# Performance work log

Measured on AMD Instinct MI355X. Metric: run time of the kernel, lower is better.

The kernel has to match this reference:

```python
import jax, jax.numpy as jnp
import numpy as np

TOPK_FALLBACK = 12  # hard-coded k in the torch source


def setup_inputs() -> dict:
    key = jax.random.key(0)
    k1, k2 = jax.random.split(key)
    bs, C, H, W = 16, 256, 128, 128
    feature_q = jax.random.normal(k1, (bs, C, H, W), dtype=jnp.float32)
    out = jax.random.normal(k2, (bs, 2, H, W), dtype=jnp.float32)
    tau = jnp.asarray(0.5, dtype=jnp.float32)  # learned threshold parameter
    return {"feature_q": feature_q, "out": out, "tau": tau}


def _proto(feat, p, thres):
    # feat: [bs, C, N], p: [bs, N] probabilities, thres: scalar
    mask = (p > thres).astype(feat.dtype)            # [bs, N]
    cnt = mask.sum(axis=-1)                          # [bs]
    # masked mean over spatial positions (single fused reduction pass)
    masked_mean = jnp.einsum('bcn,bn->bc', feat, mask) / jnp.maximum(cnt, 1.0)[:, None]
    # branchless top-k fallback when no position passes the threshold
    _, idx = jax.lax.top_k(p, TOPK_FALLBACK)         # [bs, k]
    topk_mean = jnp.take_along_axis(feat, idx[:, None, :], axis=2).mean(axis=-1)  # [bs, C]
    return jnp.where((cnt > 0)[:, None], masked_mean, topk_mean)


def reference(feature_q, out, tau):
    bs, C = feature_q.shape[0], feature_q.shape[1]
    pred = jax.nn.softmax(out.reshape(bs, 2, -1), axis=1)  # [bs, 2, N]
    pred_fg, pred_bg = pred[:, 1], pred[:, 0]
    feat = feature_q.reshape(bs, C, -1)                    # [bs, C, N]
    fg_thres = jax.nn.sigmoid(tau)
    bg_thres = 1.0 - fg_thres
    fg_proto = _proto(feat, pred_fg, fg_thres)[:, :, None, None]  # [bs, C, 1, 1]
    bg_proto = _proto(feat, pred_bg, bg_thres)[:, :, None, None]
    return fg_proto, bg_proto
```

## Files before the change

kernel.cpp:

```cpp
#include <hip/hip_runtime.h>
#include <math.h>

#define BS   16
#define CH   256
#define NPIX 16384
#define TOPK 12

__global__ __launch_bounds__(256) void mask_kernel(
    const float* __restrict__ outp,
    const float* __restrict__ tau,
    unsigned char* __restrict__ masks,
    int* __restrict__ cnts)
{
    int b = blockIdx.x >> 6;
    int n = ((blockIdx.x & 63) << 8) + threadIdx.x;

    float t = tau[0];
    float fthres = 1.0f / (1.0f + expf(-t));
    float bthres = 1.0f - fthres;

    float o0 = outp[((size_t)b * 2    ) * NPIX + n];
    float o1 = outp[((size_t)b * 2 + 1) * NPIX + n];
    float m  = fmaxf(o0, o1);
    float e0 = expf(o0 - m);
    float e1 = expf(o1 - m);
    float inv = 1.0f / (e0 + e1);
    float pf = e1 * inv;
    float pb = e0 * inv;

    int fg = pf > fthres ? 1 : 0;
    int bg = pb > bthres ? 1 : 0;
    masks[((size_t)b << 14) + n] = (unsigned char)(fg | (bg << 1));

    unsigned long long balf = __ballot(fg);
    unsigned long long balb = __ballot(bg);
    if ((threadIdx.x & 63) == 0) {
        atomicAdd(&cnts[b],      (int)__popcll(balf));
        atomicAdd(&cnts[BS + b], (int)__popcll(balb));
    }
}

__global__ __launch_bounds__(256) void sum_kernel(
    const float* __restrict__ feat,
    const unsigned char* __restrict__ masks,
    float* __restrict__ dout)
{
    int b = blockIdx.x >> 8;
    int c = blockIdx.x & (CH - 1);

    const float4* fp = (const float4*)(feat + (((size_t)b * CH + c) << 14));
    const uchar4* mp = (const uchar4*)(masks + ((size_t)b << 14));

    float sfg = 0.0f, sbg = 0.0f;
    #pragma unroll
    for (int i = 0; i < 16; ++i) {
        int idx = i * 256 + threadIdx.x;
        float4 f = fp[idx];
        uchar4 mm = mp[idx];
        if (mm.x & 1) sfg += f.x;
        if (mm.y & 1) sfg += f.y;
        if (mm.z & 1) sfg += f.z;
        if (mm.w & 1) sfg += f.w;
        if (mm.x & 2) sbg += f.x;
        if (mm.y & 2) sbg += f.y;
        if (mm.z & 2) sbg += f.z;
        if (mm.w & 2) sbg += f.w;
    }

    #pragma unroll
    for (int off = 32; off > 0; off >>= 1) {
        sfg += __shfl_down(sfg, off);
        sbg += __shfl_down(sbg, off);
    }
    __shared__ float shf[4], shb[4];
    int lane = threadIdx.x & 63, wid = threadIdx.x >> 6;
    if (lane == 0) { shf[wid] = sfg; shb[wid] = sbg; }
    __syncthreads();
    if (threadIdx.x == 0) {
        float tf = shf[0] + shf[1] + shf[2] + shf[3];
        float tb = shb[0] + shb[1] + shb[2] + shb[3];
        dout[b * CH + c]           = tf;
        dout[BS * CH + b * CH + c] = tb;
    }
}

__global__ __launch_bounds__(256) void finalize_kernel(
    const float* __restrict__ feat,
    const float* __restrict__ outp,
    const float* __restrict__ tau,
    const int* __restrict__ cnts,
    float* __restrict__ dout)
{
    int b     = blockIdx.x >> 1;
    int which = blockIdx.x & 1;
    int cnt   = cnts[which * BS + b];
    float* o  = dout + (size_t)which * BS * CH + (size_t)b * CH;

    if (cnt > 0) {
        o[threadIdx.x] = o[threadIdx.x] / (float)cnt;
        return;
    }

    __shared__ int   sel[TOPK];
    __shared__ float shv[256];
    __shared__ int   shi[256];

    const float* o0p = outp + ((size_t)b * 2) * NPIX;
    const float* o1p = o0p + NPIX;

    for (int k = 0; k < TOPK; ++k) {
        float bestv = -INFINITY;
        int   besti = 0x7fffffff;
        for (int n = threadIdx.x; n < NPIX; n += 256) {
            bool skip = false;
            for (int j = 0; j < k; ++j) if (sel[j] == n) { skip = true; break; }
            if (skip) continue;
            float a0 = o0p[n], a1 = o1p[n];
            float m  = fmaxf(a0, a1);
            float e0 = expf(a0 - m);
            float e1 = expf(a1 - m);
            float p  = (which == 0 ? e1 : e0) / (e0 + e1);
            if (p > bestv || (p == bestv && n < besti)) { bestv = p; besti = n; }
        }
        shv[threadIdx.x] = bestv;
        shi[threadIdx.x] = besti;
        __syncthreads();
        for (int off = 128; off > 0; off >>= 1) {
            if (threadIdx.x < off) {
                float v2 = shv[threadIdx.x + off];
                int   i2 = shi[threadIdx.x + off];
                if (v2 > shv[threadIdx.x] ||
                    (v2 == shv[threadIdx.x] && i2 < shi[threadIdx.x])) {
                    shv[threadIdx.x] = v2;
                    shi[threadIdx.x] = i2;
                }
            }
            __syncthreads();
        }
        if (threadIdx.x == 0) sel[k] = shi[0];
        __syncthreads();
    }

    const float* fb = feat + ((size_t)b * CH + threadIdx.x) * (size_t)NPIX;
    float s = 0.0f;
    for (int j = 0; j < TOPK; ++j) s += fb[sel[j]];
    o[threadIdx.x] = s / (float)TOPK;
}

extern "C" void kernel_launch(void* const* d_in, const int* in_sizes, int n_in,
                              void* d_out, int out_size, void* d_ws, size_t ws_size,
                              hipStream_t stream) {
    const float* feat = (const float*)d_in[0];
    const float* outp = (const float*)d_in[1];
    const float* tau  = (const float*)d_in[2];
    float* dout = (float*)d_out;

    unsigned char* masks = (unsigned char*)d_ws;
    int* cnts = (int*)((char*)d_ws + (size_t)BS * NPIX);

    hipMemsetAsync(cnts, 0, 2 * BS * sizeof(int), stream);

    mask_kernel<<<BS * (NPIX / 256), 256, 0, stream>>>(outp, tau, masks, cnts);
    sum_kernel<<<BS * CH, 256, 0, stream>>>(feat, masks, dout);
    finalize_kernel<<<2 * BS, 256, 0, stream>>>(feat, outp, tau, cnts, dout);
}
```

Before: 412.5 us.

## Pack masks into ballot bitmasks, stage in LDS, drop atomic counters

```diff
diff --git a/kernel.cpp b/kernel.cpp
--- a/kernel.cpp
+++ b/kernel.cpp
@@ -1,16 +1,20 @@
 #include <hip/hip_runtime.h>
 #include <math.h>
+#include <stdint.h>
 
 #define BS   16
 #define CH   256
 #define NPIX 16384
 #define TOPK 12
+#define WPB  (NPIX / 64)
+
+typedef float nfloat4 __attribute__((ext_vector_type(4)));
 
 __global__ __launch_bounds__(256) void mask_kernel(
     const float* __restrict__ outp,
     const float* __restrict__ tau,
-    unsigned char* __restrict__ masks,
-    int* __restrict__ cnts)
+    uint64_t* __restrict__ mfg,
+    uint64_t* __restrict__ mbg)
 {
     int b = blockIdx.x >> 6;
     int n = ((blockIdx.x & 63) << 8) + threadIdx.x;
@@ -25,46 +29,51 @@
     float e0 = expf(o0 - m);
     float e1 = expf(o1 - m);
     float inv = 1.0f / (e0 + e1);
-    float pf = e1 * inv;
-    float pb = e0 * inv;
 
-    int fg = pf > fthres ? 1 : 0;
-    int bg = pb > bthres ? 1 : 0;
-    masks[((size_t)b << 14) + n] = (unsigned char)(fg | (bg << 1));
+    int fg = (e1 * inv) > fthres;
+    int bg = (e0 * inv) > bthres;
 
-    unsigned long long balf = __ballot(fg);
-    unsigned long long balb = __ballot(bg);
+    uint64_t bf = __ballot(fg);
+    uint64_t bb = __ballot(bg);
     if ((threadIdx.x & 63) == 0) {
-        atomicAdd(&cnts[b],      (int)__popcll(balf));
-        atomicAdd(&cnts[BS + b], (int)__popcll(balb));
+        int w = n >> 6;
+        mfg[b * WPB + w] = bf;
+        mbg[b * WPB + w] = bb;
     }
 }
 
 __global__ __launch_bounds__(256) void sum_kernel(
     const float* __restrict__ feat,
-    const unsigned char* __restrict__ masks,
+    const uint64_t* __restrict__ mfg,
+    const uint64_t* __restrict__ mbg,
     float* __restrict__ dout)
 {
     int b = blockIdx.x >> 8;
     int c = blockIdx.x & (CH - 1);
 
-    const float4* fp = (const float4*)(feat + (((size_t)b * CH + c) << 14));
-    const uchar4* mp = (const uchar4*)(masks + ((size_t)b << 14));
+    __shared__ uint64_t lf[WPB], lb[WPB];
+    lf[threadIdx.x] = mfg[b * WPB + threadIdx.x];
+    lb[threadIdx.x] = mbg[b * WPB + threadIdx.x];
+    __syncthreads();
+
+    const nfloat4* fp = (const nfloat4*)(feat + (((size_t)b * CH + c) << 14));
 
     float sfg = 0.0f, sbg = 0.0f;
     #pragma unroll
     for (int i = 0; i < 16; ++i) {
         int idx = i * 256 + threadIdx.x;
-        float4 f = fp[idx];
-        uchar4 mm = mp[idx];
-        if (mm.x & 1) sfg += f.x;
-        if (mm.y & 1) sfg += f.y;
-        if (mm.z & 1) sfg += f.z;
-        if (mm.w & 1) sfg += f.w;
-        if (mm.x & 2) sbg += f.x;
-        if (mm.y & 2) sbg += f.y;
-        if (mm.z & 2) sbg += f.z;
-        if (mm.w & 2) sbg += f.w;
+        nfloat4 f = __builtin_nontemporal_load(&fp[idx]);
+        int p = idx << 2;
+        unsigned fb = (unsigned)(lf[p >> 6] >> (p & 63)) & 0xF;
+        unsigned bb = (unsigned)(lb[p >> 6] >> (p & 63)) & 0xF;
+        if (fb & 1) sfg += f.x;
+        if (fb & 2) sfg += f.y;
+        if (fb & 4) sfg += f.z;
+        if (fb & 8) sfg += f.w;
+        if (bb & 1) sbg += f.x;
+        if (bb & 2) sbg += f.y;
+        if (bb & 4) sbg += f.z;
+        if (bb & 8) sbg += f.w;
     }
 
     #pragma unroll
@@ -77,24 +86,30 @@
     if (lane == 0) { shf[wid] = sfg; shb[wid] = sbg; }
     __syncthreads();
     if (threadIdx.x == 0) {
-        float tf = shf[0] + shf[1] + shf[2] + shf[3];
-        float tb = shb[0] + shb[1] + shb[2] + shb[3];
-        dout[b * CH + c]           = tf;
-        dout[BS * CH + b * CH + c] = tb;
+        dout[b * CH + c]           = shf[0] + shf[1] + shf[2] + shf[3];
+        dout[BS * CH + b * CH + c] = shb[0] + shb[1] + shb[2] + shb[3];
     }
 }
 
 __global__ __launch_bounds__(256) void finalize_kernel(
     const float* __restrict__ feat,
     const float* __restrict__ outp,
-    const float* __restrict__ tau,
-    const int* __restrict__ cnts,
+    const uint64_t* __restrict__ mfg,
+    const uint64_t* __restrict__ mbg,
     float* __restrict__ dout)
 {
     int b     = blockIdx.x >> 1;
     int which = blockIdx.x & 1;
-    int cnt   = cnts[which * BS + b];
-    float* o  = dout + (size_t)which * BS * CH + (size_t)b * CH;
+    const uint64_t* mw = which ? mbg : mfg;
+    float* o = dout + (size_t)which * BS * CH + (size_t)b * CH;
+
+    int pc = (int)__popcll(mw[b * WPB + threadIdx.x]);
+    #pragma unroll
+    for (int off = 32; off > 0; off >>= 1) pc += __shfl_down(pc, off);
+    __shared__ int sw[4];
+    if ((threadIdx.x & 63) == 0) sw[threadIdx.x >> 6] = pc;
+    __syncthreads();
+    int cnt = sw[0] + sw[1] + sw[2] + sw[3];
 
     if (cnt > 0) {
         o[threadIdx.x] = o[threadIdx.x] / (float)cnt;
@@ -155,12 +170,10 @@
     const float* tau  = (const float*)d_in[2];
     float* dout = (float*)d_out;
 
-    unsigned char* masks = (unsigned char*)d_ws;
-    int* cnts = (int*)((char*)d_ws + (size_t)BS * NPIX);
+    uint64_t* mfg = (uint64_t*)d_ws;
+    uint64_t* mbg = (uint64_t*)((char*)d_ws + (size_t)BS * WPB * 8);
 
-    hipMemsetAsync(cnts, 0, 2 * BS * sizeof(int), stream);
-
-    mask_kernel<<<BS * (NPIX / 256), 256, 0, stream>>>(outp, tau, masks, cnts);
-    sum_kernel<<<BS * CH, 256, 0, stream>>>(feat, masks, dout);
-    finalize_kernel<<<2 * BS, 256, 0, stream>>>(feat, outp, tau, cnts, dout);
+    mask_kernel<<<BS * (NPIX / 256), 256, 0, stream>>>(outp, tau, mfg, mbg);
+    sum_kernel<<<BS * CH, 256, 0, stream>>>(feat, mfg, mbg, dout);
+    finalize_kernel<<<2 * BS, 256, 0, stream>>>(feat, outp, mfg, mbg, dout);
 }
```

After: 336.7 us. -18.4%, faster.
